# Performance work log

Measured on AMD Instinct MI355X. Metric: run time of the kernel, lower is better.

The kernel has to match this reference:

```python
import jax, jax.numpy as jnp
import numpy as np

N = 524288      # number of spacetime samples (rays*samples)
E = 16          # num_experts
K = 2           # num_selected_experts
HID = 16        # SpacetimeGeometricMLP hidden_dim (layers are hidden_dim*2 wide)
OUT = 4         # rgb + density


def setup_inputs() -> dict:
    key = jax.random.key(0)
    ks = jax.random.split(key, 8)
    return {
        "xyzt": jax.random.normal(ks[0], (N, 4), jnp.float32),
        # gate: Linear(4, E)
        "Wg": jax.random.normal(ks[1], (4, E), jnp.float32) * 0.5,
        "bg": jnp.zeros((E,), jnp.float32),
        # per-expert SphericalEmbedding params
        "proj": jax.random.normal(ks[2], (E, 3, 8), jnp.float32),
        "center": jax.random.normal(ks[3], (E, 3), jnp.float32) * 0.01,
        # per-expert TimeEmbedding biases
        "tb1": jnp.zeros((E,), jnp.float32),
        "tb2": jnp.zeros((E,), jnp.float32),
        # per-expert feature_mlp Linear(12, 2*HID, bias=False) and final Linear(2*HID, OUT)
        "W1": jax.random.normal(ks[4], (E, 12, 2 * HID), jnp.float32) * (12 ** -0.5),
        "Wf": jax.random.normal(ks[5], (E, 2 * HID, OUT), jnp.float32) * ((2 * HID) ** -0.5),
        "bf": jnp.zeros((E, OUT), jnp.float32),
    }


def _moe_forward(xyzt, Wg, bg, proj, center, tb1, tb2, W1, Wf, bf):
    n = xyzt.shape[0]
    # --- gate: top-k + softmax over selected logits (softmax in fp32, as in torch) ---
    logits = xyzt @ Wg + bg                                   # [N, E]
    w, sel = jax.lax.top_k(logits, K)                         # [N, K]
    w = jax.nn.softmax(w.astype(jnp.float32), axis=1).astype(xyzt.dtype)
    # dense combine weights: zero for unselected experts -> identical math to
    # the torch gather/scatter loop with sum pooling.
    w_dense = jnp.zeros((n, E), xyzt.dtype).at[jnp.arange(n)[:, None], sel].set(w)  # [N, E]

    xyz, t = xyzt[:, :3], xyzt[:, 3:4]

    def expert(proj_e, center_e, tb1_e, tb2_e, W1_e, Wf_e, bf_e):
        # SphericalEmbedding
        xc = xyz - center_e                                   # [N, 3]
        rho = jnp.sqrt(jnp.sum(xc * xc, -1, keepdims=True))   # [N, 1]
        phi = jnp.arctan2(xc[:, 1], xc[:, 0])[:, None]
        theta = jnp.arccos(xc[:, 2] / (rho[:, 0] + 1e-6))[:, None]
        sph = jnp.concatenate([rho, phi, theta], -1) @ proj_e  # [N, 8]
        # TimeEmbedding
        cos_t = jnp.cos(t + tb1_e)
        sin_t = jnp.sin(t + tb2_e)
        temb = jnp.concatenate([cos_t, sin_t, jax.nn.silu(cos_t), jax.nn.silu(sin_t)], -1)  # [N, 4]
        emb = jnp.concatenate([sph, temb], -1)                # [N, 12]
        # feature_mlp (depth=0, no bias) + final_layer
        h = emb @ W1_e                                        # [N, 2*HID]
        return h @ Wf_e + bf_e                                # [N, OUT]

    outs = jax.vmap(expert)(proj, center, tb1, tb2, W1, Wf, bf)  # [E, N, OUT]
    return jnp.einsum('ne,end->nd', w_dense, outs)               # [N, OUT]


def reference(xyzt, Wg, bg, proj, center, tb1, tb2, W1, Wf, bf):
    return _moe_forward(xyzt, Wg, bg, proj, center, tb1, tb2, W1, Wf, bf)
```

## Files before the change

### kernel.cpp

```cpp
#include <hip/hip_runtime.h>
#include <math.h>

#define NE 16
#define WPE 40


__global__ void moe_prep_kernel(const float* __restrict__ proj,
                                const float* __restrict__ center,
                                const float* __restrict__ tb1,
                                const float* __restrict__ tb2,
                                const float* __restrict__ W1,
                                const float* __restrict__ Wf,
                                const float* __restrict__ bf,
                                float* __restrict__ tbl) {
    int t = threadIdx.x;
    if (t >= NE * 4) return;
    int e = t >> 2, d = t & 3;

    float M[12];
    #pragma unroll
    for (int i = 0; i < 12; ++i) {
        float s = 0.f;
        const float* w1r = W1 + ((e * 12 + i) * 32);
        const float* wfc = Wf + (e * 32 * 4) + d;
        #pragma unroll
        for (int k = 0; k < 32; ++k) s = fmaf(w1r[k], wfc[k * 4], s);
        M[i] = s;
    }
    float* o = tbl + e * WPE;
    #pragma unroll
    for (int j = 0; j < 3; ++j) {
        float s = 0.f;
        const float* pr = proj + e * 24 + j * 8;
        #pragma unroll
        for (int i = 0; i < 8; ++i) s = fmaf(pr[i], M[i], s);
        o[j * 4 + d] = s;
    }
    #pragma unroll
    for (int i = 0; i < 4; ++i) o[12 + i * 4 + d] = M[8 + i];
    o[28 + d] = bf[e * 4 + d];
    if (d == 0) {
        o[32] = center[e * 3 + 0];
        o[33] = center[e * 3 + 1];
        o[34] = center[e * 3 + 2];
        o[35] = cosf(tb1[e]);
        o[36] = sinf(tb1[e]);
        o[37] = cosf(tb2[e]);
        o[38] = sinf(tb2[e]);
        o[39] = 0.f;
    }
}

__global__ __launch_bounds__(256) void moe_main_kernel(
        const float4* __restrict__ xyzt,
        const float* __restrict__ Wg,
        const float* __restrict__ bg,
        const float* __restrict__ tbl,
        float4* __restrict__ out, int n) {
    __shared__ float lds[NE * WPE];
    for (int i = threadIdx.x; i < NE * WPE; i += 256) lds[i] = tbl[i];
    __syncthreads();

    int idx = blockIdx.x * 256 + threadIdx.x;
    if (idx >= n) return;
    float4 p = xyzt[idx];

    float logits[NE];
    #pragma unroll
    for (int e = 0; e < NE; ++e) {
        logits[e] = fmaf(p.x, Wg[e],
                    fmaf(p.y, Wg[NE + e],
                    fmaf(p.z, Wg[2 * NE + e],
                    fmaf(p.w, Wg[3 * NE + e], bg[e]))));
    }
    float best = logits[0]; int bi = 0;
    float second = -INFINITY; int si = 0;
    #pragma unroll
    for (int e = 1; e < NE; ++e) {
        float l = logits[e];
        if (l > best)        { second = best; si = bi; best = l; bi = e; }
        else if (l > second) { second = l; si = e; }
    }
    float ed = expf(second - best);
    float w0 = 1.f / (1.f + ed);
    float w1 = ed * w0;

    float st, ct;
    sincosf(p.w, &st, &ct);

    int   sel[2] = { bi, si };
    float wgt[2] = { w0, w1 };
    float acc0 = 0.f, acc1 = 0.f, acc2 = 0.f, acc3 = 0.f;

    #pragma unroll
    for (int kk = 0; kk < 2; ++kk) {
        const float* w = lds + sel[kk] * WPE;
        float cx = w[32], cy = w[33], cz = w[34];
        float xc0 = p.x - cx, xc1 = p.y - cy, xc2 = p.z - cz;
        float rho = sqrtf(fmaf(xc0, xc0, fmaf(xc1, xc1, xc2 * xc2)));
        float phi = atan2f(xc1, xc0);
        float a = xc2 / (rho + 1e-6f);
        a = fminf(1.f, fmaxf(-1.f, a));
        float theta = acosf(a);
        float cos_t = fmaf(ct, w[35], -st * w[36]);
        float sin_t = fmaf(st, w[37],  ct * w[38]);
        float silc = cos_t / (1.f + expf(-cos_t));
        float sils = sin_t / (1.f + expf(-sin_t));
        float ww = wgt[kk];
        #pragma unroll
        for (int d = 0; d < 4; ++d) {
            float o = fmaf(rho,   w[0 + d],
                      fmaf(phi,   w[4 + d],
                      fmaf(theta, w[8 + d],
                      fmaf(cos_t, w[12 + d],
                      fmaf(sin_t, w[16 + d],
                      fmaf(silc,  w[20 + d],
                      fmaf(sils,  w[24 + d], w[28 + d])))))));
            if (d == 0) acc0 = fmaf(ww, o, acc0);
            if (d == 1) acc1 = fmaf(ww, o, acc1);
            if (d == 2) acc2 = fmaf(ww, o, acc2);
            if (d == 3) acc3 = fmaf(ww, o, acc3);
        }
    }
    out[idx] = make_float4(acc0, acc1, acc2, acc3);
}

extern "C" void kernel_launch(void* const* d_in, const int* in_sizes, int n_in,
                              void* d_out, int out_size, void* d_ws, size_t ws_size,
                              hipStream_t stream) {
    const float* xyzt   = (const float*)d_in[0];
    const float* Wg     = (const float*)d_in[1];
    const float* bg     = (const float*)d_in[2];
    const float* proj   = (const float*)d_in[3];
    const float* center = (const float*)d_in[4];
    const float* tb1    = (const float*)d_in[5];
    const float* tb2    = (const float*)d_in[6];
    const float* W1     = (const float*)d_in[7];
    const float* Wf     = (const float*)d_in[8];
    const float* bf     = (const float*)d_in[9];
    float* tbl = (float*)d_ws;
    int n = in_sizes[0] / 4;

    moe_prep_kernel<<<1, 64, 0, stream>>>(proj, center, tb1, tb2, W1, Wf, bf, tbl);
    moe_main_kernel<<<(n + 255) / 256, 256, 0, stream>>>(
        (const float4*)xyzt, Wg, bg, tbl, (float4*)d_out, n);
}
```

Before: 90.10 us.

## Use fast polynomial trig, vectorized LDS table reads, and parallelize prep kernel

Replaces the libm atan2f, acosf, expf and divisions with polynomial approximations, hardware reciprocal and fast intrinsics. The per-expert table is padded to 44 floats so it can be read from LDS as float4 vectors. The prep kernel now spreads the W1·Wf product over 256 threads through shared memory. The approximations lower accuracy slightly, with acos near 1e-4 absolute error, which may still sit within tolerance.

```diff
diff --git a/kernel.cpp b/kernel.cpp
--- a/kernel.cpp
+++ b/kernel.cpp
@@ -2,53 +2,96 @@
 #include <math.h>
 
 #define NE 16
-#define WPE 40
+#define WPE 44
 
 
-__global__ void moe_prep_kernel(const float* __restrict__ proj,
-                                const float* __restrict__ center,
-                                const float* __restrict__ tb1,
-                                const float* __restrict__ tb2,
-                                const float* __restrict__ W1,
-                                const float* __restrict__ Wf,
-                                const float* __restrict__ bf,
-                                float* __restrict__ tbl) {
+__global__ __launch_bounds__(256) void moe_prep_kernel(
+        const float* __restrict__ proj,
+        const float* __restrict__ center,
+        const float* __restrict__ tb1,
+        const float* __restrict__ tb2,
+        const float* __restrict__ W1,
+        const float* __restrict__ Wf,
+        const float* __restrict__ bf,
+        float* __restrict__ tbl) {
+    __shared__ float Msh[NE * 48];
     int t = threadIdx.x;
-    if (t >= NE * 4) return;
-    int e = t >> 2, d = t & 3;
+    {
+        int e = t >> 4, l = t & 15;
+        #pragma unroll
+        for (int k = 0; k < 3; ++k) {
+            int j = l + k * 16;
+            int i = j >> 2, d = j & 3;
+            const float* w1r = W1 + (e * 12 + i) * 32;
+            const float* wfc = Wf + e * 128 + d;
+            float s = 0.f;
+            #pragma unroll
+            for (int q = 0; q < 32; ++q) s = fmaf(w1r[q], wfc[q * 4], s);
+            Msh[e * 48 + j] = s;
+        }
+    }
+    __syncthreads();
+    if (t < NE * 4) {
+        int e = t >> 2, d = t & 3;
+        const float* Me = Msh + e * 48;
+        float* o = tbl + e * WPE;
+        #pragma unroll
+        for (int j = 0; j < 3; ++j) {
+            float s = 0.f;
+            const float* pr = proj + e * 24 + j * 8;
+            #pragma unroll
+            for (int i = 0; i < 8; ++i) s = fmaf(pr[i], Me[i * 4 + d], s);
+            o[j * 4 + d] = s;
+        }
+        #pragma unroll
+        for (int i = 0; i < 4; ++i) o[(3 + i) * 4 + d] = Me[(8 + i) * 4 + d];
+        o[7 * 4 + d] = bf[e * 4 + d];
+        if (d == 0) {
+            o[32] = center[e * 3 + 0];
+            o[33] = center[e * 3 + 1];
+            o[34] = center[e * 3 + 2];
+            o[35] = cosf(tb1[e]);
+            o[36] = sinf(tb1[e]);
+            o[37] = cosf(tb2[e]);
+            o[38] = sinf(tb2[e]);
+            o[39] = 0.f; o[40] = 0.f; o[41] = 0.f; o[42] = 0.f; o[43] = 0.f;
+        }
+    }
+}
 
-    float M[12];
-    #pragma unroll
-    for (int i = 0; i < 12; ++i) {
-        float s = 0.f;
-        const float* w1r = W1 + ((e * 12 + i) * 32);
-        const float* wfc = Wf + (e * 32 * 4) + d;
-        #pragma unroll
-        for (int k = 0; k < 32; ++k) s = fmaf(w1r[k], wfc[k * 4], s);
-        M[i] = s;
-    }
-    float* o = tbl + e * WPE;
-    #pragma unroll
-    for (int j = 0; j < 3; ++j) {
-        float s = 0.f;
-        const float* pr = proj + e * 24 + j * 8;
-        #pragma unroll
-        for (int i = 0; i < 8; ++i) s = fmaf(pr[i], M[i], s);
-        o[j * 4 + d] = s;
-    }
-    #pragma unroll
-    for (int i = 0; i < 4; ++i) o[12 + i * 4 + d] = M[8 + i];
-    o[28 + d] = bf[e * 4 + d];
-    if (d == 0) {
-        o[32] = center[e * 3 + 0];
-        o[33] = center[e * 3 + 1];
-        o[34] = center[e * 3 + 2];
-        o[35] = cosf(tb1[e]);
-        o[36] = sinf(tb1[e]);
-        o[37] = cosf(tb2[e]);
-        o[38] = sinf(tb2[e]);
-        o[39] = 0.f;
-    }
+__device__ __forceinline__ float fast_rcp(float x) {
+    return __builtin_amdgcn_rcpf(x);
+}
+
+__device__ __forceinline__ float4 f4fma(float s, float4 a, float4 b) {
+    return make_float4(fmaf(s, a.x, b.x), fmaf(s, a.y, b.y),
+                       fmaf(s, a.z, b.z), fmaf(s, a.w, b.w));
+}
+
+__device__ __forceinline__ float fast_atan2f(float y, float x) {
+    float ax = fabsf(x), ay = fabsf(y);
+    float mx = fmaxf(ax, ay), mn = fminf(ax, ay);
+    float r = mn * fast_rcp(fmaxf(mx, 1e-37f));
+    float s = r * r;
+    float p =              -0.0117212f;
+    p = fmaf(p, s,  0.05265332f);
+    p = fmaf(p, s, -0.11643287f);
+    p = fmaf(p, s,  0.19354346f);
+    p = fmaf(p, s, -0.33262347f);
+    p = fmaf(p, s,  0.99997726f);
+    float a = r * p;
+    a = (ay > ax) ? (1.57079637f - a) : a;
+    a = (x < 0.f) ? (3.14159274f - a) : a;
+    return copysignf(a, y);
+}
+
+__device__ __forceinline__ float fast_acosf(float x) {
+    float ax = fminf(fabsf(x), 1.f);
+    float p = fmaf(ax, -0.0187293f, 0.0742610f);
+    p = fmaf(p, ax, -0.2121144f);
+    p = fmaf(p, ax, 1.5707288f);
+    float r = sqrtf(1.f - ax) * p;
+    return (x >= 0.f) ? r : (3.14159274f - r);
 }
 
 __global__ __launch_bounds__(256) void moe_main_kernel(
@@ -81,48 +124,42 @@
         if (l > best)        { second = best; si = bi; best = l; bi = e; }
         else if (l > second) { second = l; si = e; }
     }
-    float ed = expf(second - best);
-    float w0 = 1.f / (1.f + ed);
+    float ed = __expf(second - best);
+    float w0 = fast_rcp(1.f + ed);
     float w1 = ed * w0;
 
     float st, ct;
-    sincosf(p.w, &st, &ct);
+    __sincosf(p.w, &st, &ct);
 
     int   sel[2] = { bi, si };
     float wgt[2] = { w0, w1 };
-    float acc0 = 0.f, acc1 = 0.f, acc2 = 0.f, acc3 = 0.f;
+    float4 acc = make_float4(0.f, 0.f, 0.f, 0.f);
 
     #pragma unroll
     for (int kk = 0; kk < 2; ++kk) {
-        const float* w = lds + sel[kk] * WPE;
-        float cx = w[32], cy = w[33], cz = w[34];
-        float xc0 = p.x - cx, xc1 = p.y - cy, xc2 = p.z - cz;
+        const float4* w4 = (const float4*)(lds + sel[kk] * WPE);
+        float4 cc = w4[8];
+        float4 ss = w4[9];
+        float xc0 = p.x - cc.x, xc1 = p.y - cc.y, xc2 = p.z - cc.z;
         float rho = sqrtf(fmaf(xc0, xc0, fmaf(xc1, xc1, xc2 * xc2)));
-        float phi = atan2f(xc1, xc0);
-        float a = xc2 / (rho + 1e-6f);
-        a = fminf(1.f, fmaxf(-1.f, a));
-        float theta = acosf(a);
-        float cos_t = fmaf(ct, w[35], -st * w[36]);
-        float sin_t = fmaf(st, w[37],  ct * w[38]);
-        float silc = cos_t / (1.f + expf(-cos_t));
-        float sils = sin_t / (1.f + expf(-sin_t));
-        float ww = wgt[kk];
-        #pragma unroll
-        for (int d = 0; d < 4; ++d) {
-            float o = fmaf(rho,   w[0 + d],
-                      fmaf(phi,   w[4 + d],
-                      fmaf(theta, w[8 + d],
-                      fmaf(cos_t, w[12 + d],
-                      fmaf(sin_t, w[16 + d],
-                      fmaf(silc,  w[20 + d],
-                      fmaf(sils,  w[24 + d], w[28 + d])))))));
-            if (d == 0) acc0 = fmaf(ww, o, acc0);
-            if (d == 1) acc1 = fmaf(ww, o, acc1);
-            if (d == 2) acc2 = fmaf(ww, o, acc2);
-            if (d == 3) acc3 = fmaf(ww, o, acc3);
-        }
+        float phi = fast_atan2f(xc1, xc0);
+        float theta = fast_acosf(xc2 * fast_rcp(rho + 1e-6f));
+        float cos_t = fmaf(ct, cc.w, -st * ss.x);
+        float sin_t = fmaf(st, ss.y,  ct * ss.z);
+        float silc = cos_t * fast_rcp(1.f + __expf(-cos_t));
+        float sils = sin_t * fast_rcp(1.f + __expf(-sin_t));
+
+        float4 r = w4[7];
+        r = f4fma(rho,   w4[0], r);
+        r = f4fma(phi,   w4[1], r);
+        r = f4fma(theta, w4[2], r);
+        r = f4fma(cos_t, w4[3], r);
+        r = f4fma(sin_t, w4[4], r);
+        r = f4fma(silc,  w4[5], r);
+        r = f4fma(sils,  w4[6], r);
+        acc = f4fma(wgt[kk], r, acc);
     }
-    out[idx] = make_float4(acc0, acc1, acc2, acc3);
+    out[idx] = acc;
 }
 
 extern "C" void kernel_launch(void* const* d_in, const int* in_sizes, int n_in,
@@ -141,7 +178,7 @@
     float* tbl = (float*)d_ws;
     int n = in_sizes[0] / 4;
 
-    moe_prep_kernel<<<1, 64, 0, stream>>>(proj, center, tb1, tb2, W1, Wf, bf, tbl);
+    moe_prep_kernel<<<1, 256, 0, stream>>>(proj, center, tb1, tb2, W1, Wf, bf, tbl);
     moe_main_kernel<<<(n + 255) / 256, 256, 0, stream>>>(
         (const float4*)xyzt, Wg, bg, tbl, (float4*)d_out, n);
 }
```

After: 86.29 us. 1.04x faster.
